# Optimization experiments

Hardware: AMD Instinct MI355X
Metric: run time of the kernel (lower is better)

## Reference

```python
import jax, jax.numpy as jnp
import numpy as np

# Dims from init_kwargs
B, L, D = 32, 512, 1024
NSEC = 4
SSIZE = D // NSEC          # 256
LATENT = 256
N_TOKENS = 32
BANDS = ((0, 64), (16, 128), (32, 192), (64, 256))
COEF = 0.1


def _dct_mat(N):
    # torch_dct.dct (DCT-II, unnormalized, factor 2): X[k] = 2*sum_n x[n] cos(pi*k*(2n+1)/(2N))
    n = jnp.arange(N, dtype=jnp.float32)
    k = jnp.arange(N, dtype=jnp.float32)[:, None]
    return 2.0 * jnp.cos(jnp.pi * (2.0 * n + 1.0) * k / (2.0 * N))  # [k, n]


def _idct_mat(N):
    # exact inverse of the above (DCT-III form): x[n] = (1/N)*(X[0]/2 + sum_{k>=1} X[k] cos(pi*k*(2n+1)/(2N)))
    k = jnp.arange(N, dtype=jnp.float32)
    n = jnp.arange(N, dtype=jnp.float32)[:, None]
    M = jnp.cos(jnp.pi * k * (2.0 * n + 1.0) / (2.0 * N)) / N
    return M.at[:, 0].set(1.0 / (2.0 * N))  # [n, k]


def setup_inputs() -> dict:
    key = jax.random.key(0)
    k1, k2, k3 = jax.random.split(key, 3)
    encoding = jax.random.normal(k1, (B, L, D), dtype=jnp.float32)
    W = jax.random.normal(k2, (LATENT, SSIZE), dtype=jnp.float32) / np.float32(np.sqrt(SSIZE))
    b = jax.random.normal(k3, (LATENT,), dtype=jnp.float32) * 0.01
    return {"encoding": encoding, "W": W, "b": b}


def reference(encoding, W, b):
    # encoding: [B, L, D] -> [B, L, NSEC, SSIZE]
    enc = encoding.reshape(B, L, NSEC, SSIZE)
    # Literal semantics of the torch code: H = enc[:,:,i] is [B,L,S]; H.T -> [S,L,B];
    # dct/idct act over the LAST axis (= batch), scaling indexes the seq axis.
    C = _dct_mat(B)   # [k, b]
    M = _idct_mat(B)  # [b, k]
    # DCT along batch axis for all sectors at once: [k, L, NSEC, SSIZE]
    Dk = jnp.einsum('kb,blns->klns', C, enc)
    # Per-sector band scaling along the seq axis
    seq = jnp.arange(L)
    mask = jnp.stack(
        [jnp.where((seq < lo) | (seq >= hi), jnp.float32(COEF), jnp.float32(1.0)) for (lo, hi) in BANDS],
        axis=1,
    )  # [L, NSEC]
    Dk = Dk * mask[None, :, :, None]
    # IDCT back along batch axis: [B, L, NSEC, SSIZE]
    filt = jnp.einsum('bk,klns->blns', M, Dk)
    # Linear(SSIZE -> LATENT) + tanh, then keep first N_TOKENS positions
    y = jnp.tanh(jnp.einsum('blns,os->blno', filt, W) + b)
    return y[:, :N_TOKENS]
```

## Files before the change

### kernel.cpp

```cpp
#include <hip/hip_runtime.h>
#include <math.h>

#define BATCH    32
#define LSEQ     512
#define DDIM     1024
#define NSEC     4
#define SSIZE    256
#define LATENT   256
#define NTOK     32
#define COEF     0.1f

#define ROWS     (BATCH * NTOK * NSEC)
#define COLS     LATENT
#define KDIM     SSIZE

#define TILE     64
#define BK       64
#define LDS_STRIDE 68


__global__ __launch_bounds__(256, 4)
void spectral_gemm_kernel(const float* __restrict__ enc,
                          const float* __restrict__ W,
                          const float* __restrict__ bias,
                          float* __restrict__ out) {
    __shared__ float As[BK * LDS_STRIDE];
    __shared__ float Ws[BK * LDS_STRIDE];

    const int t      = threadIdx.x;
    const int tile_r = blockIdx.x * TILE;
    const int tile_c = blockIdx.y * TILE;

    const int tx = t & 15;
    const int ty = t >> 4;

    const int sr  = t >> 2;
    const int k4b = t & 3;

    const int row_g = tile_r + sr;
    const int n = row_g & 3;
    const int l = (row_g >> 2) & 31;
    const float scale = (n == 0 || (n == 1 && l >= 16)) ? 1.0f : COEF;
    const long a_base = (long)(row_g >> 7) * (long)(LSEQ * DDIM)
                      + (long)(row_g & 127) * 256;
    const int  o_g    = tile_c + sr;

    float acc[4][4] = {{0.f,0.f,0.f,0.f},{0.f,0.f,0.f,0.f},
                       {0.f,0.f,0.f,0.f},{0.f,0.f,0.f,0.f}};

    for (int kk = 0; kk < KDIM; kk += BK) {
        #pragma unroll
        for (int it = 0; it < 4; ++it) {
            const int k4 = k4b + it * 4;
            const int kl = k4 * 4;

            float4 va = *(const float4*)&enc[a_base + kk + k4 * 4];
            va.x *= scale; va.y *= scale; va.z *= scale; va.w *= scale;
            As[(kl + 0) * LDS_STRIDE + sr] = va.x;
            As[(kl + 1) * LDS_STRIDE + sr] = va.y;
            As[(kl + 2) * LDS_STRIDE + sr] = va.z;
            As[(kl + 3) * LDS_STRIDE + sr] = va.w;

            float4 vw = *(const float4*)&W[o_g * KDIM + kk + k4 * 4];
            Ws[(kl + 0) * LDS_STRIDE + sr] = vw.x;
            Ws[(kl + 1) * LDS_STRIDE + sr] = vw.y;
            Ws[(kl + 2) * LDS_STRIDE + sr] = vw.z;
            Ws[(kl + 3) * LDS_STRIDE + sr] = vw.w;
        }
        __syncthreads();

        #pragma unroll 8
        for (int k = 0; k < BK; ++k) {
            const float4 a = *(const float4*)&As[k * LDS_STRIDE + ty * 4];
            const float4 w = *(const float4*)&Ws[k * LDS_STRIDE + tx * 4];
            acc[0][0] += a.x * w.x; acc[0][1] += a.x * w.y;
            acc[0][2] += a.x * w.z; acc[0][3] += a.x * w.w;
            acc[1][0] += a.y * w.x; acc[1][1] += a.y * w.y;
            acc[1][2] += a.y * w.z; acc[1][3] += a.y * w.w;
            acc[2][0] += a.z * w.x; acc[2][1] += a.z * w.y;
            acc[2][2] += a.z * w.z; acc[2][3] += a.z * w.w;
            acc[3][0] += a.w * w.x; acc[3][1] += a.w * w.y;
            acc[3][2] += a.w * w.z; acc[3][3] += a.w * w.w;
        }
        __syncthreads();
    }

    const float4 bv = *(const float4*)&bias[tile_c + tx * 4];
    #pragma unroll
    for (int i = 0; i < 4; ++i) {
        const int row = tile_r + ty * 4 + i;
        float4 o;
        o.x = tanhf(acc[i][0] + bv.x);
        o.y = tanhf(acc[i][1] + bv.y);
        o.z = tanhf(acc[i][2] + bv.z);
        o.w = tanhf(acc[i][3] + bv.w);
        *(float4*)&out[(long)row * COLS + tile_c + tx * 4] = o;
    }
}

extern "C" void kernel_launch(void* const* d_in, const int* in_sizes, int n_in,
                              void* d_out, int out_size, void* d_ws, size_t ws_size,
                              hipStream_t stream) {
    const float* enc  = (const float*)d_in[0];
    const float* W    = (const float*)d_in[1];
    const float* bias = (const float*)d_in[2];
    float* out = (float*)d_out;

    dim3 grid(ROWS / TILE, COLS / TILE);
    dim3 block(256);
    spectral_gemm_kernel<<<grid, block, 0, stream>>>(enc, W, bias, out);
}
```

Before: 101.5 us.

## Restructure GEMM: full-K A tile in LDS, pre-transposed W from global, fast tanh

```diff
diff --git a/kernel.cpp b/kernel.cpp
--- a/kernel.cpp
+++ b/kernel.cpp
@@ -4,96 +4,109 @@
 #define BATCH    32
 #define LSEQ     512
 #define DDIM     1024
-#define NSEC     4
 #define SSIZE    256
 #define LATENT   256
-#define NTOK     32
 #define COEF     0.1f
 
-#define ROWS     (BATCH * NTOK * NSEC)
-#define COLS     LATENT
-#define KDIM     SSIZE
+#define ROWS     4096
+#define COLS     256
+#define KDIM     256
 
-#define TILE     64
-#define BK       64
-#define LDS_STRIDE 68
+#define TR   32
+#define TC   64
+#define STR  260
 
 
-__global__ __launch_bounds__(256, 4)
+__device__ __forceinline__ float tanh_fast(float x) {
+    return 1.0f - 2.0f / (__expf(2.0f * x) + 1.0f);
+}
+
+__global__ __launch_bounds__(256, 8)
+void transpose_w_kernel(const float* __restrict__ W, float* __restrict__ Wt) {
+    __shared__ float tile[32][33];
+    const int tx = threadIdx.x;
+    const int ty = threadIdx.y;
+    const int bx = blockIdx.x;
+    const int by = blockIdx.y;
+    #pragma unroll
+    for (int i = 0; i < 4; ++i) {
+        const int o = by * 32 + ty + i * 8;
+        const int k = bx * 32 + tx;
+        tile[ty + i * 8][tx] = W[o * KDIM + k];
+    }
+    __syncthreads();
+    #pragma unroll
+    for (int i = 0; i < 4; ++i) {
+        const int k = bx * 32 + ty + i * 8;
+        const int o = by * 32 + tx;
+        Wt[k * COLS + o] = tile[tx][ty + i * 8];
+    }
+}
+
+__global__ __launch_bounds__(256, 2)
 void spectral_gemm_kernel(const float* __restrict__ enc,
-                          const float* __restrict__ W,
+                          const float* __restrict__ Wt,
                           const float* __restrict__ bias,
                           float* __restrict__ out) {
-    __shared__ float As[BK * LDS_STRIDE];
-    __shared__ float Ws[BK * LDS_STRIDE];
+    __shared__ float As[TR * STR];
 
     const int t      = threadIdx.x;
-    const int tile_r = blockIdx.x * TILE;
-    const int tile_c = blockIdx.y * TILE;
+    const int tile_r = blockIdx.x * TR;
+    const int tile_c = blockIdx.y * TC;
 
+    const float* src = enc + (long)(tile_r >> 7) * (long)(LSEQ * DDIM)
+                           + (long)(tile_r & 127) * 256;
+    #pragma unroll
+    for (int it = 0; it < 8; ++it) {
+        const int f = t + it * 256;
+        const int r = f >> 6;
+        const int k = (f & 63) << 2;
+        const float4 v = *(const float4*)(src + (long)f * 4);
+        *(float4*)&As[r * STR + k] = v;
+    }
+    __syncthreads();
+
+    const int ty = t >> 4;
     const int tx = t & 15;
-    const int ty = t >> 4;
+    const int r0 = 2 * ty;
+    const float* wp = Wt + tile_c + tx * 4;
 
-    const int sr  = t >> 2;
-    const int k4b = t & 3;
+    float acc0x = 0.f, acc0y = 0.f, acc0z = 0.f, acc0w = 0.f;
+    float acc1x = 0.f, acc1y = 0.f, acc1z = 0.f, acc1w = 0.f;
 
-    const int row_g = tile_r + sr;
-    const int n = row_g & 3;
-    const int l = (row_g >> 2) & 31;
-    const float scale = (n == 0 || (n == 1 && l >= 16)) ? 1.0f : COEF;
-    const long a_base = (long)(row_g >> 7) * (long)(LSEQ * DDIM)
-                      + (long)(row_g & 127) * 256;
-    const int  o_g    = tile_c + sr;
+    #pragma unroll 4
+    for (int k = 0; k < KDIM; k += 4) {
+        const float4 a0 = *(const float4*)&As[r0 * STR + k];
+        const float4 a1 = *(const float4*)&As[(r0 + 1) * STR + k];
+        const float4 w0 = *(const float4*)(wp + (long)(k + 0) * COLS);
+        const float4 w1 = *(const float4*)(wp + (long)(k + 1) * COLS);
+        const float4 w2 = *(const float4*)(wp + (long)(k + 2) * COLS);
+        const float4 w3 = *(const float4*)(wp + (long)(k + 3) * COLS);
 
-    float acc[4][4] = {{0.f,0.f,0.f,0.f},{0.f,0.f,0.f,0.f},
-                       {0.f,0.f,0.f,0.f},{0.f,0.f,0.f,0.f}};
+        acc0x += a0.x * w0.x; acc0y += a0.x * w0.y; acc0z += a0.x * w0.z; acc0w += a0.x * w0.w;
+        acc0x += a0.y * w1.x; acc0y += a0.y * w1.y; acc0z += a0.y * w1.z; acc0w += a0.y * w1.w;
+        acc0x += a0.z * w2.x; acc0y += a0.z * w2.y; acc0z += a0.z * w2.z; acc0w += a0.z * w2.w;
+        acc0x += a0.w * w3.x; acc0y += a0.w * w3.y; acc0z += a0.w * w3.z; acc0w += a0.w * w3.w;
 
-    for (int kk = 0; kk < KDIM; kk += BK) {
-        #pragma unroll
-        for (int it = 0; it < 4; ++it) {
-            const int k4 = k4b + it * 4;
-            const int kl = k4 * 4;
-
-            float4 va = *(const float4*)&enc[a_base + kk + k4 * 4];
-            va.x *= scale; va.y *= scale; va.z *= scale; va.w *= scale;
-            As[(kl + 0) * LDS_STRIDE + sr] = va.x;
-            As[(kl + 1) * LDS_STRIDE + sr] = va.y;
-            As[(kl + 2) * LDS_STRIDE + sr] = va.z;
-            As[(kl + 3) * LDS_STRIDE + sr] = va.w;
-
-            float4 vw = *(const float4*)&W[o_g * KDIM + kk + k4 * 4];
-            Ws[(kl + 0) * LDS_STRIDE + sr] = vw.x;
-            Ws[(kl + 1) * LDS_STRIDE + sr] = vw.y;
-            Ws[(kl + 2) * LDS_STRIDE + sr] = vw.z;
-            Ws[(kl + 3) * LDS_STRIDE + sr] = vw.w;
-        }
-        __syncthreads();
-
-        #pragma unroll 8
-        for (int k = 0; k < BK; ++k) {
-            const float4 a = *(const float4*)&As[k * LDS_STRIDE + ty * 4];
-            const float4 w = *(const float4*)&Ws[k * LDS_STRIDE + tx * 4];
-            acc[0][0] += a.x * w.x; acc[0][1] += a.x * w.y;
-            acc[0][2] += a.x * w.z; acc[0][3] += a.x * w.w;
-            acc[1][0] += a.y * w.x; acc[1][1] += a.y * w.y;
-            acc[1][2] += a.y * w.z; acc[1][3] += a.y * w.w;
-            acc[2][0] += a.z * w.x; acc[2][1] += a.z * w.y;
-            acc[2][2] += a.z * w.z; acc[2][3] += a.z * w.w;
-            acc[3][0] += a.w * w.x; acc[3][1] += a.w * w.y;
-            acc[3][2] += a.w * w.z; acc[3][3] += a.w * w.w;
-        }
-        __syncthreads();
+        acc1x += a1.x * w0.x; acc1y += a1.x * w0.y; acc1z += a1.x * w0.z; acc1w += a1.x * w0.w;
+        acc1x += a1.y * w1.x; acc1y += a1.y * w1.y; acc1z += a1.y * w1.z; acc1w += a1.y * w1.w;
+        acc1x += a1.z * w2.x; acc1y += a1.z * w2.y; acc1z += a1.z * w2.z; acc1w += a1.z * w2.w;
+        acc1x += a1.w * w3.x; acc1y += a1.w * w3.y; acc1z += a1.w * w3.z; acc1w += a1.w * w3.w;
     }
 
-    const float4 bv = *(const float4*)&bias[tile_c + tx * 4];
+    const float4 b4 = *(const float4*)&bias[tile_c + tx * 4];
+    float accs[2][4] = {{acc0x, acc0y, acc0z, acc0w}, {acc1x, acc1y, acc1z, acc1w}};
     #pragma unroll
-    for (int i = 0; i < 4; ++i) {
-        const int row = tile_r + ty * 4 + i;
+    for (int i = 0; i < 2; ++i) {
+        const int row = tile_r + r0 + i;
+        const int n = row & 3;
+        const int l = (row >> 2) & 31;
+        const float scale = (n == 0 || (n == 1 && l >= 16)) ? 1.0f : COEF;
         float4 o;
-        o.x = tanhf(acc[i][0] + bv.x);
-        o.y = tanhf(acc[i][1] + bv.y);
-        o.z = tanhf(acc[i][2] + bv.z);
-        o.w = tanhf(acc[i][3] + bv.w);
+        o.x = tanh_fast(scale * accs[i][0] + b4.x);
+        o.y = tanh_fast(scale * accs[i][1] + b4.y);
+        o.z = tanh_fast(scale * accs[i][2] + b4.z);
+        o.w = tanh_fast(scale * accs[i][3] + b4.w);
         *(float4*)&out[(long)row * COLS + tile_c + tx * 4] = o;
     }
 }
@@ -105,8 +118,10 @@
     const float* W    = (const float*)d_in[1];
     const float* bias = (const float*)d_in[2];
     float* out = (float*)d_out;
+    float* Wt  = (float*)d_ws;
 
-    dim3 grid(ROWS / TILE, COLS / TILE);
-    dim3 block(256);
-    spectral_gemm_kernel<<<grid, block, 0, stream>>>(enc, W, bias, out);
+    transpose_w_kernel<<<dim3(8, 8), dim3(32, 8), 0, stream>>>(W, Wt);
+
+    dim3 grid(ROWS / TR, COLS / TC);
+    spectral_gemm_kernel<<<grid, dim3(256), 0, stream>>>(enc, Wt, bias, out);
 }
```

Result: slower. 111.2 us (+9.6%).
